# Kernel optimization log

Measured on AMD Instinct MI355X. Metric: run time of the kernel, lower is better.

Reference implementation:

```python
import jax, jax.numpy as jnp
import numpy as np

N_QUBITS = 4  # 2x2 patch -> 4 input angles -> 4 wires, 16-amplitude state


def setup_inputs() -> dict:
    key = jax.random.key(0)
    k1, k2 = jax.random.split(key)
    x = jax.random.uniform(k1, (32, 256, 256, 1), dtype=jnp.float32)
    # RandomUniform(-0.1, 0.1) initializer, shape (n_layers, n_qubits)
    q_weights = (jax.random.uniform(k2, (2, N_QUBITS), dtype=jnp.float32) - 0.5) * 0.2
    return {"x": x, "q_weights": q_weights}


def _apply_1q(state, U, q):
    # state: (N, 2,2,2,2) complex; apply 2x2 gate U on qubit axis q+1
    axis = q + 1
    s = jnp.tensordot(U, state, axes=[[1], [axis]])  # contracted axis -> front
    return jnp.moveaxis(s, 0, axis)


def _apply_cnot(state, c, t):
    ac, at = c + 1, t + 1
    ctrl0 = jnp.take(state, 0, axis=ac)
    ctrl1 = jnp.take(state, 1, axis=ac)
    at_r = at - 1 if at > ac else at  # target axis index after removing control axis
    ctrl1 = jnp.flip(ctrl1, axis=at_r)  # flip target when control=1
    return jnp.stack([ctrl0, ctrl1], axis=ac)


def reference(x, q_weights):
    B, H, W, _ = x.shape
    oh, ow = H // 2, W // 2
    # 2x2 stride-2 patch extraction, row-major within patch (matches tf.image.extract_patches)
    patches = x.reshape(B, oh, 2, ow, 2).transpose(0, 1, 3, 2, 4).reshape(-1, N_QUBITS)
    # RY(inputs * pi/2) on |0>: amplitudes [cos(theta/2), sin(theta/2)], theta/2 = inputs*pi/4
    ang = patches * np.float32(np.pi / 4)
    v = jnp.stack([jnp.cos(ang), jnp.sin(ang)], axis=-1).astype(jnp.complex64)  # (N, 4, 2)
    state = jnp.einsum('ni,nj,nk,nl->nijkl', v[:, 0], v[:, 1], v[:, 2], v[:, 3])  # (N,2,2,2,2)

    n_layers = q_weights.shape[0]
    for l in range(n_layers):
        for q in range(N_QUBITS):
            c = jnp.cos(q_weights[l, q] * 0.5).astype(jnp.complex64)
            s = jnp.sin(q_weights[l, q] * 0.5).astype(jnp.complex64)
            # RX(w) = [[cos(w/2), -i sin(w/2)], [-i sin(w/2), cos(w/2)]]
            U = jnp.stack([jnp.stack([c, -1j * s]), jnp.stack([-1j * s, c])])
            state = _apply_1q(state, U, q)
        for q in range(N_QUBITS):
            state = _apply_cnot(state, q, (q + 1) % N_QUBITS)

    probs = state.real ** 2 + state.imag ** 2  # (N,2,2,2,2) float32
    all_axes = (1, 2, 3, 4)
    zs = []
    for q in range(N_QUBITS):
        other = tuple(a for a in all_axes if a != q + 1)
        marg = probs.sum(axis=other)  # (N, 2)
        zs.append(marg[:, 0] - marg[:, 1])  # <Z_q>
    out = jnp.stack(zs, axis=-1)  # (N, 4)
    return out.reshape(B, oh, ow, N_QUBITS)
```

## Files before the change

### kernel.cpp

```cpp
#include <hip/hip_runtime.h>


__global__ __launch_bounds__(256) void qlayer_kernel(
    const float* __restrict__ x,
    const float* __restrict__ qw,
    float* __restrict__ out,
    int n_total)
{
    int n = blockIdx.x * blockDim.x + threadIdx.x;
    if (n >= n_total) return;

    int ow = n & 127;
    int oh = (n >> 7) & 127;
    int b  = n >> 14;

    const float* row0 = x + ((size_t)(b * 256 + 2 * oh) * 256 + 2 * ow);
    const float* row1 = row0 + 256;
    float2 p0 = *(const float2*)row0;
    float2 p1 = *(const float2*)row1;

    const float PI_4 = 0.78539816339744830962f;
    float ang[4] = { p0.x * PI_4, p0.y * PI_4, p1.x * PI_4, p1.y * PI_4 };

    float vc[4], vs[4];
#pragma unroll
    for (int q = 0; q < 4; ++q) {
        __sincosf(ang[q], &vs[q], &vc[q]);
    }

    float re[16], im[16];
#pragma unroll
    for (int i = 0; i < 2; ++i) {
        float v0 = i ? vs[0] : vc[0];
#pragma unroll
        for (int j = 0; j < 2; ++j) {
            float v01 = v0 * (j ? vs[1] : vc[1]);
#pragma unroll
            for (int k = 0; k < 2; ++k) {
                float v012 = v01 * (k ? vs[2] : vc[2]);
#pragma unroll
                for (int l = 0; l < 2; ++l) {
                    int m = i * 8 + j * 4 + k * 2 + l;
                    re[m] = v012 * (l ? vs[3] : vc[3]);
                    im[m] = 0.0f;
                }
            }
        }
    }

    float gc[8], gs[8];
#pragma unroll
    for (int i = 0; i < 8; ++i) {
        __sincosf(qw[i] * 0.5f, &gs[i], &gc[i]);
    }

#pragma unroll
    for (int l = 0; l < 2; ++l) {
#pragma unroll
        for (int q = 0; q < 4; ++q) {
            float c = gc[l * 4 + q];
            float s = gs[l * 4 + q];
            int mask = 8 >> q;
#pragma unroll
            for (int m = 0; m < 16; ++m) {
                if (m & mask) continue;
                int m1 = m | mask;
                float r0 = re[m],  i0 = im[m];
                float r1 = re[m1], i1 = im[m1];
                re[m]  = c * r0 + s * i1;
                im[m]  = c * i0 - s * r1;
                re[m1] = c * r1 + s * i0;
                im[m1] = c * i1 - s * r0;
            }
        }
#pragma unroll
        for (int q = 0; q < 4; ++q) {
            int t = (q + 1) & 3;
            int cmask = 8 >> q;
            int tmask = 8 >> t;
#pragma unroll
            for (int m = 0; m < 16; ++m) {
                if (!(m & cmask) || (m & tmask)) continue;
                int m1 = m ^ tmask;
                float tr = re[m]; re[m] = re[m1]; re[m1] = tr;
                float ti = im[m]; im[m] = im[m1]; im[m1] = ti;
            }
        }
    }

    float p[16];
#pragma unroll
    for (int m = 0; m < 16; ++m) {
        p[m] = re[m] * re[m] + im[m] * im[m];
    }

    float z[4];
#pragma unroll
    for (int q = 0; q < 4; ++q) {
        int mask = 8 >> q;
        float acc = 0.0f;
#pragma unroll
        for (int m = 0; m < 16; ++m) {
            acc += (m & mask) ? -p[m] : p[m];
        }
        z[q] = acc;
    }

    float4 o = make_float4(z[0], z[1], z[2], z[3]);
    *(float4*)(out + (size_t)n * 4) = o;
}

extern "C" void kernel_launch(void* const* d_in, const int* in_sizes, int n_in,
                              void* d_out, int out_size, void* d_ws, size_t ws_size,
                              hipStream_t stream) {
    const float* x  = (const float*)d_in[0];
    const float* qw = (const float*)d_in[1];
    float* out = (float*)d_out;
    int n_total = out_size / 4;
    dim3 block(256);
    dim3 grid((n_total + 255) / 256);
    hipLaunchKernelGGL(qlayer_kernel, grid, block, 0, stream, x, qw, out, n_total);
}
```

Baseline: 71.36 us.

## Replace statevector simulation with closed-form expectation expressions

Drops the 16-amplitude complex statevector simulation and computes each Z expectation with a hand-derived closed-form product of per-qubit cos/sin terms. It also switches to the hardware sin/cos instructions, which take arguments in revolutions. The goal is to remove nearly all arithmetic, but the kernel is likely memory-bound, so the gain may be small. The derivation is hard to check and is prone to algebra mistakes.

```diff
diff --git a/kernel.cpp b/kernel.cpp
--- a/kernel.cpp
+++ b/kernel.cpp
@@ -15,99 +15,78 @@
     int b  = n >> 14;
 
     const float* row0 = x + ((size_t)(b * 256 + 2 * oh) * 256 + 2 * ow);
-    const float* row1 = row0 + 256;
     float2 p0 = *(const float2*)row0;
-    float2 p1 = *(const float2*)row1;
+    float2 p1 = *(const float2*)(row0 + 256);
 
-    const float PI_4 = 0.78539816339744830962f;
-    float ang[4] = { p0.x * PI_4, p0.y * PI_4, p1.x * PI_4, p1.y * PI_4 };
-
-    float vc[4], vs[4];
+    float xv[4] = { p0.x, p0.y, p1.x, p1.y };
+    float Cth[4], Sth[4];
 #pragma unroll
-    for (int q = 0; q < 4; ++q) {
-        __sincosf(ang[q], &vs[q], &vc[q]);
+    for (int j = 0; j < 4; ++j) {
+        float r = xv[j] * 0.25f;
+        Sth[j] = __builtin_amdgcn_sinf(r);
+        Cth[j] = __builtin_amdgcn_cosf(r);
     }
 
-    float re[16], im[16];
+    const float INV2PI = 0.15915494309189535f;
+    float C1[4], S1[4], C2[4], S2[4];
 #pragma unroll
-    for (int i = 0; i < 2; ++i) {
-        float v0 = i ? vs[0] : vc[0];
-#pragma unroll
-        for (int j = 0; j < 2; ++j) {
-            float v01 = v0 * (j ? vs[1] : vc[1]);
-#pragma unroll
-            for (int k = 0; k < 2; ++k) {
-                float v012 = v01 * (k ? vs[2] : vc[2]);
-#pragma unroll
-                for (int l = 0; l < 2; ++l) {
-                    int m = i * 8 + j * 4 + k * 2 + l;
-                    re[m] = v012 * (l ? vs[3] : vc[3]);
-                    im[m] = 0.0f;
-                }
-            }
-        }
+    for (int j = 0; j < 4; ++j) {
+        float r1 = qw[j]     * INV2PI;
+        float r2 = qw[4 + j] * INV2PI;
+        S1[j] = __builtin_amdgcn_sinf(r1);
+        C1[j] = __builtin_amdgcn_cosf(r1);
+        S2[j] = __builtin_amdgcn_sinf(r2);
+        C2[j] = __builtin_amdgcn_cosf(r2);
     }
 
-    float gc[8], gs[8];
+    float gz[4], gy[4], X[4];
 #pragma unroll
-    for (int i = 0; i < 8; ++i) {
-        __sincosf(qw[i] * 0.5f, &gs[i], &gc[i]);
+    for (int j = 0; j < 4; ++j) {
+        gz[j] = C1[j] * Cth[j];
+        gy[j] = -S1[j] * Cth[j];
+        X[j]  = Sth[j];
     }
 
-#pragma unroll
-    for (int l = 0; l < 2; ++l) {
-#pragma unroll
-        for (int q = 0; q < 4; ++q) {
-            float c = gc[l * 4 + q];
-            float s = gs[l * 4 + q];
-            int mask = 8 >> q;
-#pragma unroll
-            for (int m = 0; m < 16; ++m) {
-                if (m & mask) continue;
-                int m1 = m | mask;
-                float r0 = re[m],  i0 = im[m];
-                float r1 = re[m1], i1 = im[m1];
-                re[m]  = c * r0 + s * i1;
-                im[m]  = c * i0 - s * r1;
-                re[m1] = c * r1 + s * i0;
-                im[m1] = c * i1 - s * r0;
-            }
-        }
-#pragma unroll
-        for (int q = 0; q < 4; ++q) {
-            int t = (q + 1) & 3;
-            int cmask = 8 >> q;
-            int tmask = 8 >> t;
-#pragma unroll
-            for (int m = 0; m < 16; ++m) {
-                if (!(m & cmask) || (m & tmask)) continue;
-                int m1 = m ^ tmask;
-                float tr = re[m]; re[m] = re[m1]; re[m1] = tr;
-                float ti = im[m]; im[m] = im[m1]; im[m1] = ti;
-            }
-        }
-    }
+    float a0  = C2[0] * gz[0];
+    float b0  = S2[0] * gy[0];
+    float in1 = fmaf(b0, X[1], a0);
+    float in2 = fmaf(a0, X[1], b0);
+    float z1  = gz[3] * fmaf(S2[1] * gy[2], in2, C2[1] * gz[2] * in1);
 
-    float p[16];
-#pragma unroll
-    for (int m = 0; m < 16; ++m) {
-        p[m] = re[m] * re[m] + im[m] * im[m];
-    }
+    float m23a = X[2] * gz[3];
+    float m23b = X[2] * gy[3];
+    float P = fmaf(S2[2], m23b,  C2[2] * gz[3]);
+    float R = fmaf(C2[2], m23a,  S2[2] * gy[3]);
+    float Q = fmaf(S2[2], m23a, -C2[2] * gy[3]);
+    float T = fmaf(C2[2], m23b, -S2[2] * gz[3]);
 
-    float z[4];
-#pragma unroll
-    for (int q = 0; q < 4; ++q) {
-        int mask = 8 >> q;
-        float acc = 0.0f;
-#pragma unroll
-        for (int m = 0; m < 16; ++m) {
-            acc += (m & mask) ? -p[m] : p[m];
-        }
-        z[q] = acc;
-    }
+    float u1 = C2[1] * gz[1], u2 = S2[1] * gy[1];
+    float u3 = C2[1] * gy[1], u4 = S2[1] * gz[1];
+    float M1 = fmaf(u2, R, u1 * P);
+    float M2 = fmaf(u4, T, u3 * Q);
+    float M3 = fmaf(-u4, R, u3 * P);
 
-    float4 o = make_float4(z[0], z[1], z[2], z[3]);
-    *(float4*)(out + (size_t)n * 4) = o;
+    float z0 = fmaf(S2[3] * gy[0], M2, C2[3] * gz[0] * M1);
+    float z2 = fmaf(S2[0] * X[0], M3, C2[0] * M1);
+
+    float m2a = X[3] * gz[2];
+    float m2b = X[3] * gy[2];
+    float U  = fmaf(S2[2], m2b,  C2[2] * gz[2]);
+    float V  = fmaf(C2[2], m2a,  S2[2] * gy[2]);
+    float W  = fmaf(-S2[2], m2a, C2[2] * gy[2]);
+    float Xp = fmaf(C2[2], m2b, -S2[2] * gz[2]);
+
+    float cc = C2[0] * C2[3], ss = S2[0] * S2[3];
+    float cs = C2[0] * S2[3], sc = S2[0] * C2[3];
+    float A  = fmaf(-ss, V,  cc * U);
+    float Bq = fmaf(-ss, Xp, cc * W);
+    float D  = fmaf(sc, W,  cs * Xp);
+    float E  = fmaf(sc, U,  cs * V);
+    float t1 = fmaf(S2[1] * X[1], Bq, C2[1] * A);
+    float t2 = fmaf(C2[1] * X[1], E,  S2[1] * D);
+    float z3 = fmaf(gy[0], t2, gz[0] * t1);
+
+    *(float4*)(out + (size_t)n * 4) = make_float4(z0, z1, z2, z3);
 }
 
 extern "C" void kernel_launch(void* const* d_in, const int* in_sizes, int n_in,
```

After: 61.73 us. 1.16x faster.
